# Optimization experiments

Measured on AMD Instinct MI355X. Metric: run time of the kernel, lower is better.

The kernel has to match this reference:

```python
import jax, jax.numpy as jnp
import numpy as np
from jax import lax

B, T, D = 16, 800, 80
HOP = 256          # hop_size
WIN = 512          # window_size = 2*hop
FFT = 1024         # fft_size
CCH = 256          # conv_channels
OUT = 222          # ltv_out_channels
GRP = 8            # group_size


def _conv1d_same(h, W, b, groups=1):
    # h: (B, C, T); W: (O, C//groups, 3). torch Conv1d pads (k-1)*d=2 then slices
    # [pad//2 : -pad//2], which is exactly SAME padding (1,1) for k=3, d=1.
    y = lax.conv_general_dilated(h, W, (1,), [(1, 1)], feature_group_count=groups,
                                 dimension_numbers=('NCH', 'OIH', 'NCH'))
    return y + b[None, :, None]


def setup_inputs() -> dict:
    key = jax.random.key(0)
    ks = jax.random.split(key, 8)
    s = 0.02  # small weight scale keeps 10**(Re(FFT)/10) numerically sane
    x = jax.random.normal(ks[0], (B, T, D), jnp.float32)
    z = 0.1 * jax.random.normal(ks[1], (B, 1, T * HOP), jnp.float32)
    W1 = s * jax.random.normal(ks[2], (CCH, D, 3), jnp.float32)
    b1 = jnp.zeros((CCH,), jnp.float32)
    W2 = s * jax.random.normal(ks[3], (CCH, CCH // GRP, 3), jnp.float32)
    b2 = jnp.zeros((CCH,), jnp.float32)
    W3 = s * jax.random.normal(ks[4], (CCH, CCH // GRP, 3), jnp.float32)
    b3 = jnp.zeros((CCH,), jnp.float32)
    W4 = s * jax.random.normal(ks[5], (OUT, CCH, 3), jnp.float32)
    b4 = jnp.zeros((OUT,), jnp.float32)
    return dict(x=x, z=z, W1=W1, b1=b1, W2=W2, b2=b2, W3=W3, b3=b3, W4=W4, b4=b4)


def _forward(x, z, W1, b1, W2, b2, W3, b3, W4, b4):
    # --- ConvLayers (original_conv): conv/relu stack over time axis ---
    h = x.transpose(0, 2, 1)                          # (B, D, T)
    h = jax.nn.relu(_conv1d_same(h, W1, b1))
    h = jax.nn.relu(_conv1d_same(h, W2, b2, GRP))
    h = jax.nn.relu(_conv1d_same(h, W3, b3, GRP))
    ccep = _conv1d_same(h, W4, b4).transpose(0, 2, 1)  # (B, T, 222)
    # quefrency norm: [111,...,1, 1,...,111]
    idx = jnp.arange(1, OUT // 2 + 1, dtype=ccep.dtype)
    quef = jnp.concatenate([idx[::-1], idx])
    ccep = ccep / quef

    # --- _ccep2impulse: cepstrum -> impulse response via FFT ---
    pad = (FFT - OUT) // 2                            # 401
    Y = jnp.fft.fft(jnp.pad(ccep, ((0, 0), (0, 0), (pad, pad))), n=FFT, axis=-1)
    mag = 10.0 ** (Y.real / 10.0)
    imp = jnp.fft.ifft(mag * jnp.exp(1j * Y.imag), n=FFT, axis=-1).real  # (B,T,1024)

    # --- _conv_impulse: per-frame time-varying convolution ---
    zp = jnp.pad(z.reshape(B, -1), ((0, 0), (WIN // 2 - 1, WIN // 2)))   # (B, L+511)
    fidx = jnp.arange(T)[:, None] * HOP + jnp.arange(WIN)[None, :]
    frames = zp[:, fidx]                                                 # (B, T, 512)
    fp = jnp.pad(frames, ((0, 0), (0, 0), (FFT // 2 - 1, FFT // 2)))     # (B, T, 1535)
    # out[n] = sum_k fp[n+k] * imp[k]  (valid cross-correlation, 512 outputs).
    # Realize as circular correlation with N=2048 >= 1534+512 (no wraparound).
    N = 2048
    C = jnp.fft.irfft(jnp.fft.rfft(fp, N) * jnp.conj(jnp.fft.rfft(imp, N)), N)[..., :WIN]

    # --- _ola: window + overlap-add ---
    n = jnp.arange(WIN, dtype=C.dtype)
    win = 0.5 * (1.0 - jnp.cos(2.0 * jnp.pi * n / WIN))  # periodic hann, win_norm=1
    zw = C * win                                          # (B, T, 512)
    ola = zw[..., :HOP] + jnp.roll(zw[..., HOP:], 1, axis=1)
    return jnp.clip(ola.reshape(B, 1, T * HOP), -1.0, 1.0)


def reference(x, z, W1, b1, W2, b2, W3, b3, W4, b4):
    return _forward(x, z, W1, b1, W2, b2, W3, b3, W4, b4)
```

## Files before the change

kernel.cpp:

```cpp
#include <hip/hip_runtime.h>
#include <hip/hip_bf16.h>

#define T_LEN 800
#define B_SZ  16
#define D_IN  80
#define CCH   256
#define OUT_CH 222
#define HOPSZ 256
#define WINSZ 512
#define ZLEN  (T_LEN*HOPSZ)
#define CSTRIDE 256

#define PHI(i) ((i) + ((i)>>3))

typedef short short8 __attribute__((ext_vector_type(8)));
typedef float f32x4 __attribute__((ext_vector_type(4)));

__device__ __forceinline__ float2 cmul(float2 a, float2 b){
    return make_float2(a.x*b.x - a.y*b.y, a.x*b.y + a.y*b.x);
}

__global__ __launch_bounds__(256) void k_wtrans(const float* __restrict__ W1,
                                                const float* __restrict__ W2,
                                                const float* __restrict__ W3,
                                                const float* __restrict__ W4,
                                                float4* __restrict__ w1t,
                                                float4* __restrict__ w2t,
                                                float4* __restrict__ w3t,
                                                __hip_bfloat16* __restrict__ wfhi,
                                                __hip_bfloat16* __restrict__ wflo){
    const int i = blockIdx.x*256 + threadIdx.x;
    switch (blockIdx.y){
    case 0: if (i < 80*256){
        int ci = i >> 8, co = i & 255;
        const float* s = &W1[(co*80 + ci)*3];
        w1t[i] = make_float4(s[0], s[1], s[2], 0.f);
    } break;
    case 1: if (i < 32*256){
        int cil = i >> 8, co = i & 255;
        const float* s = &W2[(co*32 + cil)*3];
        w2t[i] = make_float4(s[0], s[1], s[2], 0.f);
    } break;
    case 2: if (i < 32*256){
        int cil = i >> 8, co = i & 255;
        const float* s = &W3[(co*32 + cil)*3];
        w3t[i] = make_float4(s[0], s[1], s[2], 0.f);
    } break;
    default: if (i < 768*256){
        int k = i >> 8, co = i & 255;
        int d = k >> 8, ci = k & 255;
        float w = 0.f;
        if (co < OUT_CH){
            float q = (co < 111) ? (float)(111 - co) : (float)(co - 110);
            w = W4[(co*256 + ci)*3 + d] / q;
        }
        __hip_bfloat16 h = __float2bfloat16(w);
        __hip_bfloat16 l = __float2bfloat16(w - __bfloat162float(h));
        int kt = k >> 5, g = (k >> 3) & 3, e = k & 7;
        int idx = ((kt*4 + g)*256 + co)*8 + e;
        wfhi[idx] = h;
        wflo[idx] = l;
    } break;
    }
}

__global__ __launch_bounds__(256) void k_conv123(const float* __restrict__ x,
                                                 const float4* __restrict__ W1t,
                                                 const float* __restrict__ b1,
                                                 const float4* __restrict__ W2t,
                                                 const float* __restrict__ b2,
                                                 const float4* __restrict__ W3t,
                                                 const float* __restrict__ b3,
                                                 __hip_bfloat16* __restrict__ ohi,
                                                 __hip_bfloat16* __restrict__ olo){
    __shared__ __align__(16) float xs[80*24];
    __shared__ __align__(16) float hs[256*20];
    const int t0 = blockIdx.x * 16;
    const int b  = blockIdx.y;
    const int tid = threadIdx.x;
    const int co = tid;
    const int gbase = (co >> 5) << 5;
    for (int i = tid; i < 80*22; i += 256){
        int tt = i / 80, ci = i - tt*80;
        int t = t0 - 3 + tt;
        xs[ci*24 + tt] = (t >= 0 && t < T_LEN) ? x[(b*T_LEN + t)*D_IN + ci] : 0.f;
    }
    __syncthreads();
    {
        float acc[20];
        float bv = b1[co];
        #pragma unroll
        for (int j = 0; j < 20; ++j) acc[j] = bv;
        const float4* wp = W1t + co;
        float4 w = *wp;
        for (int ci = 0; ci < 80; ++ci){
            wp += 256;
            float4 wn = *wp;
            const float* xp = &xs[ci*24];
            float4 v0 = *(const float4*)(xp);
            float4 v1 = *(const float4*)(xp + 4);
            float4 v2 = *(const float4*)(xp + 8);
            float4 v3 = *(const float4*)(xp + 12);
            float4 v4 = *(const float4*)(xp + 16);
            float2 v5 = *(const float2*)(xp + 20);
            float xr[22] = {v0.x,v0.y,v0.z,v0.w, v1.x,v1.y,v1.z,v1.w,
                            v2.x,v2.y,v2.z,v2.w, v3.x,v3.y,v3.z,v3.w,
                            v4.x,v4.y,v4.z,v4.w, v5.x,v5.y};
            #pragma unroll
            for (int j = 0; j < 20; ++j){
                acc[j] = fmaf(xr[j],   w.x, acc[j]);
                acc[j] = fmaf(xr[j+1], w.y, acc[j]);
                acc[j] = fmaf(xr[j+2], w.z, acc[j]);
            }
            w = wn;
        }
        #pragma unroll
        for (int j = 0; j < 20; ++j){
            int t = t0 - 2 + j;
            hs[co*20 + j] = (t >= 0 && t < T_LEN) ? fmaxf(acc[j], 0.f) : 0.f;
        }
    }
    __syncthreads();
    float acc2[18];
    {
        float bv = b2[co];
        #pragma unroll
        for (int j = 0; j < 18; ++j) acc2[j] = bv;
        const float4* wp = W2t + co;
        float4 w = *wp;
        for (int cil = 0; cil < 32; ++cil){
            wp += 256;
            float4 wn = *wp;
            const float* xp = &hs[(gbase + cil)*20];
            float4 v0 = *(const float4*)(xp);
            float4 v1 = *(const float4*)(xp + 4);
            float4 v2 = *(const float4*)(xp + 8);
            float4 v3 = *(const float4*)(xp + 12);
            float4 v4 = *(const float4*)(xp + 16);
            float xr[20] = {v0.x,v0.y,v0.z,v0.w, v1.x,v1.y,v1.z,v1.w,
                            v2.x,v2.y,v2.z,v2.w, v3.x,v3.y,v3.z,v3.w,
                            v4.x,v4.y,v4.z,v4.w};
            #pragma unroll
            for (int j = 0; j < 18; ++j){
                acc2[j] = fmaf(xr[j],   w.x, acc2[j]);
                acc2[j] = fmaf(xr[j+1], w.y, acc2[j]);
                acc2[j] = fmaf(xr[j+2], w.z, acc2[j]);
            }
            w = wn;
        }
    }
    __syncthreads();
    #pragma unroll
    for (int j = 0; j < 18; ++j){
        int t = t0 - 1 + j;
        hs[co*20 + j] = (t >= 0 && t < T_LEN) ? fmaxf(acc2[j], 0.f) : 0.f;
    }
    __syncthreads();
    float acc3[16];
    {
        float bv = b3[co];
        #pragma unroll
        for (int j = 0; j < 16; ++j) acc3[j] = bv;
        const float4* wp = W3t + co;
        float4 w = *wp;
        for (int cil = 0; cil < 32; ++cil){
            wp += 256;
            float4 wn = *wp;
            const float* xp = &hs[(gbase + cil)*20];
            float4 v0 = *(const float4*)(xp);
            float4 v1 = *(const float4*)(xp + 4);
            float4 v2 = *(const float4*)(xp + 8);
            float4 v3 = *(const float4*)(xp + 12);
            float2 v4 = *(const float2*)(xp + 16);
            float xr[18] = {v0.x,v0.y,v0.z,v0.w, v1.x,v1.y,v1.z,v1.w,
                            v2.x,v2.y,v2.z,v2.w, v3.x,v3.y,v3.z,v3.w, v4.x,v4.y};
            #pragma unroll
            for (int j = 0; j < 16; ++j){
                acc3[j] = fmaf(xr[j],   w.x, acc3[j]);
                acc3[j] = fmaf(xr[j+1], w.y, acc3[j]);
                acc3[j] = fmaf(xr[j+2], w.z, acc3[j]);
            }
            w = wn;
        }
    }
    #pragma unroll
    for (int j = 0; j < 16; ++j){
        float v = fmaxf(acc3[j], 0.f);
        __hip_bfloat16 h = __float2bfloat16(v);
        __hip_bfloat16 l = __float2bfloat16(v - __bfloat162float(h));
        size_t idx = (size_t)(b*T_LEN + t0 + j)*CCH + co;
        ohi[idx] = h;
        olo[idx] = l;
    }
}

__global__ __launch_bounds__(256) void k_conv4(const __hip_bfloat16* __restrict__ hhi,
                                               const __hip_bfloat16* __restrict__ hlo,
                                               const __hip_bfloat16* __restrict__ wfhi,
                                               const __hip_bfloat16* __restrict__ wflo,
                                               const float* __restrict__ bias,
                                               float* __restrict__ ccep){
    __shared__ __align__(16) unsigned char aLds[2][34*512];
    const int gx = blockIdx.x;
    const int b  = gx / 25;
    const int t0 = (gx - b*25) * 32;
    const int coBase = blockIdx.y << 7;
    const int tid = threadIdx.x;
    const int wave = tid >> 6;
    const int l = tid & 63;
    const int l15 = l & 15, lg = l >> 4;

    for (int i = tid; i < 2*1088; i += 256){
        int p = (i >= 1088);
        int c = i - (p ? 1088 : 0);
        int r = c >> 5, c16 = c & 31;
        int t = t0 - 1 + r;
        uint4 v = make_uint4(0u,0u,0u,0u);
        if (t >= 0 && t < T_LEN){
            const __hip_bfloat16* src = (p ? hlo : hhi) + (((size_t)(b*T_LEN + t)) << 8) + (c16 << 3);
            v = *(const uint4*)src;
        }
        int off = (r << 9) + (c16 << 4);
        off ^= (r & 7) << 4;
        *(uint4*)(&aLds[p][off]) = v;
    }
    __syncthreads();

    const int co0 = coBase + (wave << 5);
    f32x4 acc[2][2];
    #pragma unroll
    for (int n = 0; n < 2; ++n){
        int co = co0 + (n << 4) + l15;
        float bq = 0.f;
        if (co < OUT_CH){
            float q = (co < 111) ? (float)(111 - co) : (float)(co - 110);
            bq = bias[co] / q;
        }
        acc[0][n] = f32x4{bq, bq, bq, bq};
        acc[1][n] = f32x4{bq, bq, bq, bq};
    }

    for (int kt = 0; kt < 24; ++kt){
        const int d   = kt >> 3;
        const int cib = (kt & 7) << 6;
        short8 ah[2], al[2];
        #pragma unroll
        for (int m = 0; m < 2; ++m){
            int r = l15 + d + (m << 4);
            int off = (r << 9) + cib + (lg << 4);
            off ^= (r & 7) << 4;
            ah[m] = __builtin_bit_cast(short8, *(const uint4*)(&aLds[0][off]));
            al[m] = __builtin_bit_cast(short8, *(const uint4*)(&aLds[1][off]));
        }
        #pragma unroll
        for (int n = 0; n < 2; ++n){
            int co = co0 + (n << 4) + l15;
            size_t woff = ((size_t)((kt << 2) + lg) << 8) + co;
            short8 bh = __builtin_bit_cast(short8, *(const uint4*)(wfhi + (woff << 3)));
            short8 bl = __builtin_bit_cast(short8, *(const uint4*)(wflo + (woff << 3)));
            #pragma unroll
            for (int m = 0; m < 2; ++m){
                acc[m][n] = __builtin_amdgcn_mfma_f32_16x16x32_bf16(ah[m], bh, acc[m][n], 0, 0, 0);
                acc[m][n] = __builtin_amdgcn_mfma_f32_16x16x32_bf16(ah[m], bl, acc[m][n], 0, 0, 0);
                acc[m][n] = __builtin_amdgcn_mfma_f32_16x16x32_bf16(al[m], bh, acc[m][n], 0, 0, 0);
            }
        }
    }

    #pragma unroll
    for (int m = 0; m < 2; ++m){
        #pragma unroll
        for (int n = 0; n < 2; ++n){
            int co = co0 + (n << 4) + l15;
            #pragma unroll
            for (int j = 0; j < 4; ++j){
                int t = t0 + (m << 4) + (lg << 2) + j;
                ccep[((size_t)(b*T_LEN + t) << 8) + co] = acc[m][n][j];
            }
        }
    }
}

template<int N4, int Ns, bool INV, bool SKIP3>
__device__ __forceinline__ void r4s(const float2* __restrict__ src,
                                    float2* __restrict__ dst,
                                    const float2* __restrict__ Wt,
                                    int j){
    const int jm = j & (Ns - 1);
    float2 v0 = src[PHI(j)];
    float2 v1 = src[PHI(j + N4)];
    float2 v2 = src[PHI(j + 2*N4)];
    float2 v3 = make_float2(0.f, 0.f);
    if (!SKIP3) v3 = src[PHI(j + 3*N4)];
    if (Ns > 1){
        const int e = jm * (256 / Ns);
        float2 w1 = Wt[PHI(e)];
        if (INV) w1.y = -w1.y;
        float2 w2 = cmul(w1, w1);
        float2 w3 = cmul(w2, w1);
        v1 = cmul(v1, w1);
        v2 = cmul(v2, w2);
        if (!SKIP3) v3 = cmul(v3, w3);
    }
    float2 t0 = make_float2(v0.x + v2.x, v0.y + v2.y);
    float2 t1 = make_float2(v0.x - v2.x, v0.y - v2.y);
    float2 t2, t3;
    if (SKIP3){ t2 = v1; t3 = v1; }
    else {
        t2 = make_float2(v1.x + v3.x, v1.y + v3.y);
        t3 = make_float2(v1.x - v3.x, v1.y - v3.y);
    }
    float2 o0 = make_float2(t0.x + t2.x, t0.y + t2.y);
    float2 o2 = make_float2(t0.x - t2.x, t0.y - t2.y);
    float2 o1, o3;
    if (!INV){
        o1 = make_float2(t1.x + t3.y, t1.y - t3.x);
        o3 = make_float2(t1.x - t3.y, t1.y + t3.x);
    } else {
        o1 = make_float2(t1.x - t3.y, t1.y + t3.x);
        o3 = make_float2(t1.x + t3.y, t1.y - t3.x);
    }
    const int base = ((j - jm) << 2) + jm;
    dst[PHI(base)]          = o0;
    dst[PHI(base + Ns)]     = o1;
    dst[PHI(base + 2*Ns)]   = o2;
    dst[PHI(base + 3*Ns)]   = o3;
}

__global__ __launch_bounds__(256) void k_filter(const float* __restrict__ ccep,
                                                const float* __restrict__ z,
                                                float* __restrict__ zw){
    __shared__ __align__(16) float2 A[1152];
    __shared__ __align__(16) float2 Bb[1152];
    __shared__ __align__(16) float2 Wt[576];
    const int t = blockIdx.x;
    const int b = blockIdx.y;
    const int tid = threadIdx.x;
    const float PI2 = 6.283185307179586f;

    for (int j = tid; j < 512; j += 256){
        float s, c;
        __sincosf(-PI2 * (float)j * (1.0f/1024.0f), &s, &c);
        Wt[PHI(j)] = make_float2(c, s);
    }
    const float* crow = &ccep[(b*T_LEN + t)*CSTRIDE];
    #pragma unroll
    for (int r = 0; r < 4; ++r){
        int i = tid + (r << 8);
        float av = (i >= 401 && i < 623) ? crow[i - 401] : 0.f;
        float fv = 0.f;
        if (i < 512){
            int zi = t*HOPSZ + i - 255;
            fv = (zi >= 0 && zi < ZLEN) ? z[b*ZLEN + zi] : 0.f;
        }
        A[PHI(i)] = make_float2(av, fv);
    }
    __syncthreads();

    r4s<256,1,  false,true >(A,  Bb, Wt, tid); __syncthreads();
    r4s<256,4,  false,false>(Bb, A,  Wt, tid); __syncthreads();
    r4s<256,16, false,false>(A,  Bb, Wt, tid); __syncthreads();
    r4s<256,64, false,false>(Bb, A,  Wt, tid); __syncthreads();
    r4s<256,256,false,false>(A,  Bb, Wt, tid); __syncthreads();

    {
        const float LOG2_10_DIV10 = 0.33219280948873623f;
        auto unpackG = [&](int i)->float2 {
            float2 P = Bb[PHI(i)];
            float2 Q = Bb[PHI((1024 - i) & 1023)];
            float Are = 0.5f * (P.x + Q.x);
            float Aim = 0.5f * (P.y - Q.y);
            float Fx  = 0.5f * (P.y + Q.y);
            float Fy  = 0.5f * (Q.x - P.x);
            float mag = exp2f(Are * LOG2_10_DIV10) * (1.0f/1024.0f);
            float s, c;
            __sincosf(Aim, &s, &c);
            float Hx = mag * c, Hy = mag * s;
            return make_float2(Fx*Hx + Fy*Hy, Fx*Hy - Fy*Hx);
        };
        int k = tid;
        float2 G  = unpackG(k);
        float2 G2 = unpackG(512 - k);
        float sx = G.x + G2.x, sy = G.y - G2.y;
        float dx = G.x - G2.x, dy = G.y + G2.y;
        float2 V = Wt[PHI(k)];
        float ux = dx*V.x + dy*V.y;
        float uy = dy*V.x - dx*V.y;
        A[PHI(k)] = make_float2(sx - uy, sy + ux);
        if (k){
            A[PHI(512 - k)] = make_float2(sx + uy, ux - sy);
        } else {
            float2 G3 = unpackG(256);
            A[PHI(256)] = make_float2(2.f*G3.x, -2.f*G3.y);
        }
    }
    __syncthreads();

    if (tid < 128) r4s<128,1, true,false>(A,  Bb, Wt, tid);
    __syncthreads();
    if (tid < 128) r4s<128,4, true,false>(Bb, A,  Wt, tid);
    __syncthreads();
    if (tid < 128) r4s<128,16,true,false>(A,  Bb, Wt, tid);
    __syncthreads();
    if (tid < 128) r4s<128,64,true,false>(Bb, A,  Wt, tid);
    __syncthreads();
    {
        int j = tid;
        float2 u = A[PHI(j)];
        float2 v = A[PHI(j + 256)];
        float2 w = Wt[PHI(2*j)];
        w.y = -w.y;
        float2 vv = cmul(v, w);
        Bb[PHI(j)]       = make_float2(u.x + vv.x, u.y + vv.y);
        Bb[PHI(j + 256)] = make_float2(u.x - vv.x, u.y - vv.y);
    }
    __syncthreads();

    float* zrow = &zw[(size_t)(b*T_LEN + t)*512];
    #pragma unroll
    for (int r = 0; r < 2; ++r){
        int n = tid + (r << 8);
        int m = (511 - n) >> 1;
        float2 zv = Bb[PHI(m)];
        float yv = (n & 1) ? zv.x : zv.y;
        float wv = 0.5f * (1.0f - __cosf(PI2 * (float)n * (1.0f/512.0f)));
        zrow[n] = yv * wv;
    }
}

__global__ __launch_bounds__(256) void k_ola(const float* __restrict__ zw,
                                             float* __restrict__ out){
    const int t = blockIdx.x;
    const int b = blockIdx.y;
    const int h = threadIdx.x;
    const int tm = (t + T_LEN - 1) % T_LEN;
    float v = zw[(size_t)(b*T_LEN + t)*512 + h]
            + zw[(size_t)(b*T_LEN + tm)*512 + 256 + h];
    v = fminf(fmaxf(v, -1.0f), 1.0f);
    out[(size_t)b*ZLEN + t*HOPSZ + h] = v;
}

extern "C" void kernel_launch(void* const* d_in, const int* in_sizes, int n_in,
                              void* d_out, int out_size, void* d_ws, size_t ws_size,
                              hipStream_t stream){
    const float* x  = (const float*)d_in[0];
    const float* z  = (const float*)d_in[1];
    const float* W1 = (const float*)d_in[2];
    const float* b1 = (const float*)d_in[3];
    const float* W2 = (const float*)d_in[4];
    const float* b2 = (const float*)d_in[5];
    const float* W3 = (const float*)d_in[6];
    const float* b3 = (const float*)d_in[7];
    const float* W4 = (const float*)d_in[8];
    const float* b4 = (const float*)d_in[9];
    float* out = (float*)d_out;
    float* ws  = (float*)d_ws;

    float* ccep = ws;
    __hip_bfloat16* h3hi = (__hip_bfloat16*)(ws + 3276800);
    __hip_bfloat16* h3lo = h3hi + 3276800;
    float* zwb  = ws + 6553600;
    float4* w1t = (float4*)(zwb);
    float4* w2t = (float4*)(zwb + 81920);
    float4* w3t = (float4*)(zwb + 114688);
    __hip_bfloat16* wfhi = (__hip_bfloat16*)(zwb + 147456);
    __hip_bfloat16* wflo = wfhi + 196608;

    dim3 blk(256);
    dim3 gwt(768, 4);
    dim3 gconv(T_LEN/16, B_SZ);
    dim3 gc4(400, 2);
    dim3 gf(T_LEN, B_SZ);

    k_wtrans<<<gwt, blk, 0, stream>>>(W1, W2, W3, W4, w1t, w2t, w3t, wfhi, wflo);
    k_conv123<<<gconv, blk, 0, stream>>>(x, w1t, b1, w2t, b2, w3t, b3, h3hi, h3lo);
    k_conv4<<<gc4, blk, 0, stream>>>(h3hi, h3lo, wfhi, wflo, b4, ccep);
    k_filter<<<gf, blk, 0, stream>>>(ccep, z, zwb);
    k_ola<<<gf, blk, 0, stream>>>(zwb, out);
}
```

Measured before the change: 154.1 us.

## Move first conv layer onto bf16x3 MFMA with split-precision weights and inputs

Replaces the scalar FP32 FMA loop of the first conv (80->256 channels, k=3) with 16x16x32 bf16 MFMA instructions. It uses a hi/lo bf16 split (three MFMAs per tile) to keep near-fp32 accuracy. Weights are pre-packed in the transform kernel into an MFMA-friendly layout padded to 96 input channels. Input is staged in shared memory as hi/lo bf16 rows. The aim is to cut the ALU cost of conv1. The cost is padding waste and extra MFMA passes, and the gain is limited because conv1 is only a small part of the whole pipeline.

```diff
diff --git a/kernel.cpp b/kernel.cpp
--- a/kernel.cpp
+++ b/kernel.cpp
@@ -10,6 +10,7 @@
 #define WINSZ 512
 #define ZLEN  (T_LEN*HOPSZ)
 #define CSTRIDE 256
+#define XSTR 104
 
 #define PHI(i) ((i) + ((i)>>3))
 
@@ -24,27 +25,36 @@
                                                 const float* __restrict__ W2,
                                                 const float* __restrict__ W3,
                                                 const float* __restrict__ W4,
-                                                float4* __restrict__ w1t,
                                                 float4* __restrict__ w2t,
                                                 float4* __restrict__ w3t,
+                                                __hip_bfloat16* __restrict__ w1fhi,
+                                                __hip_bfloat16* __restrict__ w1flo,
                                                 __hip_bfloat16* __restrict__ wfhi,
                                                 __hip_bfloat16* __restrict__ wflo){
     const int i = blockIdx.x*256 + threadIdx.x;
     switch (blockIdx.y){
-    case 0: if (i < 80*256){
-        int ci = i >> 8, co = i & 255;
-        const float* s = &W1[(co*80 + ci)*3];
-        w1t[i] = make_float4(s[0], s[1], s[2], 0.f);
-    } break;
-    case 1: if (i < 32*256){
+    case 0: if (i < 32*256){
         int cil = i >> 8, co = i & 255;
         const float* s = &W2[(co*32 + cil)*3];
         w2t[i] = make_float4(s[0], s[1], s[2], 0.f);
     } break;
-    case 2: if (i < 32*256){
+    case 1: if (i < 32*256){
         int cil = i >> 8, co = i & 255;
         const float* s = &W3[(co*32 + cil)*3];
         w3t[i] = make_float4(s[0], s[1], s[2], 0.f);
+    } break;
+    case 2: if (i < 9*4*256*8){
+        int e  = i & 7;
+        int co = (i >> 3) & 255;
+        int lg = (i >> 11) & 3;
+        int dk = i >> 13;
+        int d  = dk / 3, kt = dk - 3*d;
+        int ci = kt*32 + lg*8 + e;
+        float w = (ci < 80) ? W1[(co*80 + ci)*3 + d] : 0.f;
+        __hip_bfloat16 h = __float2bfloat16(w);
+        __hip_bfloat16 l = __float2bfloat16(w - __bfloat162float(h));
+        w1fhi[i] = h;
+        w1flo[i] = l;
     } break;
     default: if (i < 768*256){
         int k = i >> 8, co = i & 255;
@@ -65,7 +75,8 @@
 }
 
 __global__ __launch_bounds__(256) void k_conv123(const float* __restrict__ x,
-                                                 const float4* __restrict__ W1t,
+                                                 const __hip_bfloat16* __restrict__ w1fhi,
+                                                 const __hip_bfloat16* __restrict__ w1flo,
                                                  const float* __restrict__ b1,
                                                  const float4* __restrict__ W2t,
                                                  const float* __restrict__ b2,
@@ -73,54 +84,84 @@
                                                  const float* __restrict__ b3,
                                                  __hip_bfloat16* __restrict__ ohi,
                                                  __hip_bfloat16* __restrict__ olo){
-    __shared__ __align__(16) float xs[80*24];
+    __shared__ __align__(16) __hip_bfloat16 xhi[34*XSTR];
+    __shared__ __align__(16) __hip_bfloat16 xlo[34*XSTR];
     __shared__ __align__(16) float hs[256*20];
     const int t0 = blockIdx.x * 16;
     const int b  = blockIdx.y;
     const int tid = threadIdx.x;
     const int co = tid;
     const int gbase = (co >> 5) << 5;
-    for (int i = tid; i < 80*22; i += 256){
-        int tt = i / 80, ci = i - tt*80;
-        int t = t0 - 3 + tt;
-        xs[ci*24 + tt] = (t >= 0 && t < T_LEN) ? x[(b*T_LEN + t)*D_IN + ci] : 0.f;
-    }
-    __syncthreads();
+    const int wave = tid >> 6;
+    const int l = tid & 63;
+    const int l15 = l & 15, lg4 = l >> 4;
+
+    for (int i = tid; i < 34*XSTR; i += 256){
+        int rr = i / XSTR, c = i - rr*XSTR;
+        float v = 0.f;
+        if (c < 80){
+            int t = t0 - 3 + rr;
+            v = (t >= 0 && t < T_LEN) ? x[(b*T_LEN + t)*D_IN + c] : 0.f;
+        }
+        __hip_bfloat16 h = __float2bfloat16(v);
+        xhi[i] = h;
+        xlo[i] = __float2bfloat16(v - __bfloat162float(h));
+    }
+    __syncthreads();
+
     {
-        float acc[20];
-        float bv = b1[co];
-        #pragma unroll
-        for (int j = 0; j < 20; ++j) acc[j] = bv;
-        const float4* wp = W1t + co;
-        float4 w = *wp;
-        for (int ci = 0; ci < 80; ++ci){
-            wp += 256;
-            float4 wn = *wp;
-            const float* xp = &xs[ci*24];
-            float4 v0 = *(const float4*)(xp);
-            float4 v1 = *(const float4*)(xp + 4);
-            float4 v2 = *(const float4*)(xp + 8);
-            float4 v3 = *(const float4*)(xp + 12);
-            float4 v4 = *(const float4*)(xp + 16);
-            float2 v5 = *(const float2*)(xp + 20);
-            float xr[22] = {v0.x,v0.y,v0.z,v0.w, v1.x,v1.y,v1.z,v1.w,
-                            v2.x,v2.y,v2.z,v2.w, v3.x,v3.y,v3.z,v3.w,
-                            v4.x,v4.y,v4.z,v4.w, v5.x,v5.y};
+        f32x4 acc1[2][4];
+        #pragma unroll
+        for (int n = 0; n < 4; ++n){
+            float bv = b1[(wave << 6) + (n << 4) + l15];
+            acc1[0][n] = f32x4{bv, bv, bv, bv};
+            acc1[1][n] = f32x4{bv, bv, bv, bv};
+        }
+        #pragma unroll
+        for (int d = 0; d < 3; ++d){
             #pragma unroll
-            for (int j = 0; j < 20; ++j){
-                acc[j] = fmaf(xr[j],   w.x, acc[j]);
-                acc[j] = fmaf(xr[j+1], w.y, acc[j]);
-                acc[j] = fmaf(xr[j+2], w.z, acc[j]);
+            for (int kt = 0; kt < 3; ++kt){
+                short8 ah[2], al[2];
+                #pragma unroll
+                for (int m = 0; m < 2; ++m){
+                    int off = ((m << 4) + l15 + d)*XSTR + kt*32 + lg4*8;
+                    ah[m] = __builtin_bit_cast(short8, *(const uint4*)(xhi + off));
+                    al[m] = __builtin_bit_cast(short8, *(const uint4*)(xlo + off));
+                }
+                #pragma unroll
+                for (int n = 0; n < 4; ++n){
+                    int co_n = (wave << 6) + (n << 4) + l15;
+                    int wo = ((((d*3 + kt)*4 + lg4) << 8) + co_n) << 3;
+                    short8 bh = __builtin_bit_cast(short8, *(const uint4*)(w1fhi + wo));
+                    short8 bl = __builtin_bit_cast(short8, *(const uint4*)(w1flo + wo));
+                    #pragma unroll
+                    for (int m = 0; m < 2; ++m){
+                        acc1[m][n] = __builtin_amdgcn_mfma_f32_16x16x32_bf16(ah[m], bh, acc1[m][n], 0, 0, 0);
+                        acc1[m][n] = __builtin_amdgcn_mfma_f32_16x16x32_bf16(ah[m], bl, acc1[m][n], 0, 0, 0);
+                        acc1[m][n] = __builtin_amdgcn_mfma_f32_16x16x32_bf16(al[m], bh, acc1[m][n], 0, 0, 0);
+                    }
+                }
             }
-            w = wn;
-        }
-        #pragma unroll
-        for (int j = 0; j < 20; ++j){
-            int t = t0 - 2 + j;
-            hs[co*20 + j] = (t >= 0 && t < T_LEN) ? fmaxf(acc[j], 0.f) : 0.f;
-        }
-    }
-    __syncthreads();
+        }
+        #pragma unroll
+        for (int m = 0; m < 2; ++m){
+            #pragma unroll
+            for (int n = 0; n < 4; ++n){
+                int co_n = (wave << 6) + (n << 4) + l15;
+                #pragma unroll
+                for (int j = 0; j < 4; ++j){
+                    int trow = (m << 4) + (lg4 << 2) + j;
+                    if (trow < 20){
+                        int t = t0 - 2 + trow;
+                        float v = (t >= 0 && t < T_LEN) ? fmaxf(acc1[m][n][j], 0.f) : 0.f;
+                        hs[co_n*20 + trow] = v;
+                    }
+                }
+            }
+        }
+    }
+    __syncthreads();
+
     float acc2[18];
     {
         float bv = b2[co];
@@ -460,11 +501,12 @@
     __hip_bfloat16* h3hi = (__hip_bfloat16*)(ws + 3276800);
     __hip_bfloat16* h3lo = h3hi + 3276800;
     float* zwb  = ws + 6553600;
-    float4* w1t = (float4*)(zwb);
-    float4* w2t = (float4*)(zwb + 81920);
-    float4* w3t = (float4*)(zwb + 114688);
-    __hip_bfloat16* wfhi = (__hip_bfloat16*)(zwb + 147456);
-    __hip_bfloat16* wflo = wfhi + 196608;
+    float4* w2t = (float4*)(zwb);
+    float4* w3t = (float4*)(zwb + 32768);
+    __hip_bfloat16* w1fhi = (__hip_bfloat16*)(zwb + 65536);
+    __hip_bfloat16* w1flo = (__hip_bfloat16*)(zwb + 102400);
+    __hip_bfloat16* wfhi  = (__hip_bfloat16*)(zwb + 139264);
+    __hip_bfloat16* wflo  = (__hip_bfloat16*)(zwb + 237568);
 
     dim3 blk(256);
     dim3 gwt(768, 4);
@@ -472,8 +514,8 @@
     dim3 gc4(400, 2);
     dim3 gf(T_LEN, B_SZ);
 
-    k_wtrans<<<gwt, blk, 0, stream>>>(W1, W2, W3, W4, w1t, w2t, w3t, wfhi, wflo);
-    k_conv123<<<gconv, blk, 0, stream>>>(x, w1t, b1, w2t, b2, w3t, b3, h3hi, h3lo);
+    k_wtrans<<<gwt, blk, 0, stream>>>(W1, W2, W3, W4, w2t, w3t, w1fhi, w1flo, wfhi, wflo);
+    k_conv123<<<gconv, blk, 0, stream>>>(x, w1fhi, w1flo, b1, w2t, b2, w3t, b3, h3hi, h3lo);
     k_conv4<<<gc4, blk, 0, stream>>>(h3hi, h3lo, wfhi, wflo, b4, ccep);
     k_filter<<<gf, blk, 0, stream>>>(ccep, z, zwb);
     k_ola<<<gf, blk, 0, stream>>>(zwb, out);
```

Result: faster. 144.0 us, median of 2 (-6.6%).
